# Kernel optimization log

Hardware: AMD Instinct MI355X
Metric: run time of the kernel (lower is better)

Reference implementation:

```python
import jax, jax.numpy as jnp
import numpy as np

D_MODEL = 1024
NUM_HEADS = 16
D_K = D_MODEL // NUM_HEADS
ROPE_THETA = 10000.0
SEQ = 4096


def setup_inputs() -> dict:
    key = jax.random.key(0)
    ks = jax.random.split(key, 5)
    s = 1.0 / np.sqrt(D_MODEL)
    return {
        "x": jax.random.normal(ks[0], (1, SEQ, D_MODEL), jnp.float32),
        "token_positions": jnp.arange(SEQ, dtype=jnp.int32),
        "Wq": jax.random.normal(ks[1], (D_MODEL, D_MODEL), jnp.float32) * s,
        "Wk": jax.random.normal(ks[2], (D_MODEL, D_MODEL), jnp.float32) * s,
        "Wv": jax.random.normal(ks[3], (D_MODEL, D_MODEL), jnp.float32) * s,
        "Wo": jax.random.normal(ks[4], (D_MODEL, D_MODEL), jnp.float32) * s,
    }


def _rope(t, positions):
    # t: [b, h, s, d_k]; interleaved pair rotation
    half = D_K // 2
    inv_freq = ROPE_THETA ** (-jnp.arange(half, dtype=jnp.float32) * 2.0 / D_K)
    ang = positions.astype(jnp.float32)[:, None] * inv_freq[None, :]  # [s, half]
    cos, sin = jnp.cos(ang), jnp.sin(ang)
    x1 = t[..., 0::2]
    x2 = t[..., 1::2]
    r1 = x1 * cos - x2 * sin
    r2 = x1 * sin + x2 * cos
    return jnp.stack([r1, r2], axis=-1).reshape(t.shape)


def reference(x, token_positions, Wq, Wk, Wv, Wo):
    b, s, _ = x.shape
    def split_heads(t):
        return t.reshape(b, s, NUM_HEADS, D_K).transpose(0, 2, 1, 3)  # [b,h,s,dk]
    q = split_heads(x @ Wq.T)
    k = split_heads(x @ Wk.T)
    v = split_heads(x @ Wv.T)
    q = _rope(q, token_positions)
    k = _rope(k, token_positions)
    scores = jnp.einsum('bhqd,bhkd->bhqk', q, k) / np.sqrt(D_K)
    causal = jnp.tril(jnp.ones((s, s), dtype=bool))
    scores = jnp.where(causal, scores, -jnp.inf)
    attn = jax.nn.softmax(scores, axis=-1)
    out = jnp.einsum('bhqk,bhkd->bhqd', attn, v)
    out = out.transpose(0, 2, 1, 3).reshape(b, s, D_MODEL)
    return out @ Wo.T
```

## Files before the change

### kernel.cpp

```cpp
#include <hip/hip_runtime.h>

#define S    4096
#define DM   1024
#define H    16
#define DK   64

typedef __bf16 bf16;
typedef __bf16 bf16x8 __attribute__((ext_vector_type(8)));
typedef __bf16 bf16x4 __attribute__((ext_vector_type(4)));
typedef float  f32x4  __attribute__((ext_vector_type(4)));

__global__ __launch_bounds__(256)
void convert_kernel(const float* __restrict__ x,  const float* __restrict__ wq,
                    const float* __restrict__ wk, const float* __restrict__ wv,
                    const float* __restrict__ wo,
                    bf16* __restrict__ xb,  bf16* __restrict__ wqb,
                    bf16* __restrict__ wkb, bf16* __restrict__ wvb,
                    bf16* __restrict__ wob)
{
    const size_t i = (size_t)blockIdx.x * 256 + threadIdx.x;
    const float* src; bf16* dst; size_t off;
    if (i < 1048576)      { src = x;  dst = xb;  off = i; }
    else if (i < 1310720) { src = wq; dst = wqb; off = i - 1048576; }
    else if (i < 1572864) { src = wk; dst = wkb; off = i - 1310720; }
    else if (i < 1835008) { src = wv; dst = wvb; off = i - 1572864; }
    else                  { src = wo; dst = wob; off = i - 1835008; }
    f32x4 v = ((const f32x4*)src)[off];
    bf16x4 b;
    for (int r = 0; r < 4; r++) b[r] = (bf16)v[r];
    ((bf16x4*)dst)[off] = b;
}

__global__ __launch_bounds__(256)
void gemm_kernel(const bf16* __restrict__ A,
                 const bf16* __restrict__ w0, const bf16* __restrict__ w1,
                 const bf16* __restrict__ w2,
                 const int* __restrict__ pos,
                 bf16* __restrict__ o0, bf16* __restrict__ o1,
                 bf16* __restrict__ o2,
                 float* __restrict__ of,
                 int base_mode)
{
    const int z    = blockIdx.z;
    const int mode = base_mode + z;
    const bf16* W  = (z == 0) ? w0 : (z == 1 ? w1 : w2);
    bf16* Out      = (z == 0) ? o0 : (z == 1 ? o1 : o2);

    __shared__ bf16 As[64 * 72];
    __shared__ bf16 Bs[64 * 72];

    const int tid  = threadIdx.x;
    const int lane = tid & 63;
    const int wv   = tid >> 6;
    const int quad = lane >> 4;
    const int col  = lane & 15;
    const int wm   = wv >> 1, wn = wv & 1;

    const int tileM = blockIdx.x * 64;
    const int tileN = blockIdx.y * 64;

    const int ldRow = tid >> 2;
    const int ldK   = (tid & 3) * 16;

    f32x4 acc[2][2] = {};

    for (int kc = 0; kc < DM; kc += 64) {
        bf16x8 a0 = *(const bf16x8*)&A[(size_t)(tileM + ldRow) * DM + kc + ldK];
        bf16x8 a1 = *(const bf16x8*)&A[(size_t)(tileM + ldRow) * DM + kc + ldK + 8];
        bf16x8 b0 = *(const bf16x8*)&W[(size_t)(tileN + ldRow) * DM + kc + ldK];
        bf16x8 b1 = *(const bf16x8*)&W[(size_t)(tileN + ldRow) * DM + kc + ldK + 8];
        __syncthreads();
        *(bf16x8*)&As[ldRow * 72 + ldK]     = a0;
        *(bf16x8*)&As[ldRow * 72 + ldK + 8] = a1;
        *(bf16x8*)&Bs[ldRow * 72 + ldK]     = b0;
        *(bf16x8*)&Bs[ldRow * 72 + ldK + 8] = b1;
        __syncthreads();

        for (int kk = 0; kk < 2; kk++) {
            bf16x8 af0 = *(const bf16x8*)&As[(wm * 32 + 0 * 16 + col) * 72 + kk * 32 + quad * 8];
            bf16x8 af1 = *(const bf16x8*)&As[(wm * 32 + 1 * 16 + col) * 72 + kk * 32 + quad * 8];
            bf16x8 bf0 = *(const bf16x8*)&Bs[(wn * 32 + 0 * 16 + col) * 72 + kk * 32 + quad * 8];
            bf16x8 bf1 = *(const bf16x8*)&Bs[(wn * 32 + 1 * 16 + col) * 72 + kk * 32 + quad * 8];

            acc[0][0] = __builtin_amdgcn_mfma_f32_16x16x32_bf16(af0, bf0, acc[0][0], 0, 0, 0);
            acc[0][1] = __builtin_amdgcn_mfma_f32_16x16x32_bf16(af0, bf1, acc[0][1], 0, 0, 0);
            acc[1][0] = __builtin_amdgcn_mfma_f32_16x16x32_bf16(af1, bf0, acc[1][0], 0, 0, 0);
            acc[1][1] = __builtin_amdgcn_mfma_f32_16x16x32_bf16(af1, bf1, acc[1][1], 0, 0, 0);
        }
    }

    for (int fm = 0; fm < 2; fm++)
    for (int fn = 0; fn < 2; fn++) {
        f32x4 v = acc[fm][fn];
        const int n = tileN + wn * 32 + fn * 16 + col;
        for (int r = 0; r < 4; r++) {
            const int m = tileM + wm * 32 + fm * 16 + quad * 4 + r;
            float val = v[r];
            if (mode <= 1) {
                float part = __shfl_xor(val, 1);
                const int d = n & 63;
                const int i = d >> 1;
                float inv = exp2f(-(float)i * 0.41524101186092034f);
                float ang = (float)pos[m] * inv;
                float c = cosf(ang), sn = sinf(ang);
                float rot = (n & 1) ? (val * c + part * sn)
                                    : (val * c - part * sn);
                if (mode == 0) rot *= 0.18033688011112042f;
                Out[((size_t)(n >> 6) * S + m) * 64 + d] = (bf16)rot;
            } else if (mode == 2) {
                Out[(size_t)n * S + m] = (bf16)val;
            } else {
                of[(size_t)m * DM + n] = val;
            }
        }
    }
}

__global__ __launch_bounds__(256, 5)
void attn_kernel(const bf16* __restrict__ q, const bf16* __restrict__ k,
                 const bf16* __restrict__ vt,
                 bf16* __restrict__ P0g, bf16* __restrict__ P1g,
                 float* __restrict__ l0g, float* __restrict__ l1g)
{
    const int bx   = blockIdx.x;
    const int qb_  = (bx & 1) ? (63 - (bx >> 1)) : (bx >> 1);
    const int h    = blockIdx.y;
    const int z    = blockIdx.z;
    const int tid  = threadIdx.x;
    const int lane = tid & 63;
    const int wv   = tid >> 6;
    const int quad = lane >> 4;
    const int col  = lane & 15;

    const int nt   = qb_ + 1;
    const int half = (nt + 1) >> 1;
    const int kt0  = z ? half : 0;
    const int kt1  = z ? nt   : half;

    __shared__ bf16 Ks[64 * 72];
    __shared__ bf16 Vs[64 * 72];
    __shared__ bf16 plds[4][16 * 72];

    const int qbase = qb_ * 64 + wv * 16;

    bf16x8 qf0 = *(const bf16x8*)&q[((size_t)(h * S + qbase + col)) * 64 + quad * 8];
    bf16x8 qf1 = *(const bf16x8*)&q[((size_t)(h * S + qbase + col)) * 64 + 32 + quad * 8];

    float li = 0.f;
    f32x4 o[4] = {};
    const int gq = qbase + col;

    const int srow = tid >> 2;
    const int sseg = (tid & 3) * 16;
    const bf16* kg_ = k  + ((size_t)h * S) * 64;
    const bf16* vg_ = vt + ((size_t)h * 64) * S;

    bf16x8 kr0 = *(const bf16x8*)(kg_ + (size_t)(kt0 * 64 + srow) * 64 + sseg);
    bf16x8 kr1 = *(const bf16x8*)(kg_ + (size_t)(kt0 * 64 + srow) * 64 + sseg + 8);
    bf16x8 vr0 = *(const bf16x8*)(vg_ + (size_t)srow * S + kt0 * 64 + sseg);
    bf16x8 vr1 = *(const bf16x8*)(vg_ + (size_t)srow * S + kt0 * 64 + sseg + 8);

    for (int kt = kt0; kt < kt1; kt++) {
        const int kbase = kt * 64;

        __syncthreads();
        *(bf16x8*)&Ks[srow * 72 + sseg]     = kr0;
        *(bf16x8*)&Ks[srow * 72 + sseg + 8] = kr1;
        *(bf16x8*)&Vs[srow * 72 + sseg]     = vr0;
        *(bf16x8*)&Vs[srow * 72 + sseg + 8] = vr1;
        __syncthreads();

        if (kt + 1 < kt1) {
            const int nb = kbase + 64;
            kr0 = *(const bf16x8*)(kg_ + (size_t)(nb + srow) * 64 + sseg);
            kr1 = *(const bf16x8*)(kg_ + (size_t)(nb + srow) * 64 + sseg + 8);
            vr0 = *(const bf16x8*)(vg_ + (size_t)srow * S + nb + sseg);
            vr1 = *(const bf16x8*)(vg_ + (size_t)srow * S + nb + sseg + 8);
        }

        f32x4 st[4];
        __builtin_amdgcn_s_setprio(1);
        for (int kg = 0; kg < 4; kg++) {
            bf16x8 kf0 = *(const bf16x8*)&Ks[(kg * 16 + col) * 72 + quad * 8];
            bf16x8 kf1 = *(const bf16x8*)&Ks[(kg * 16 + col) * 72 + 32 + quad * 8];
            f32x4 zz = {};
            zz = __builtin_amdgcn_mfma_f32_16x16x32_bf16(kf0, qf0, zz, 0, 0, 0);
            zz = __builtin_amdgcn_mfma_f32_16x16x32_bf16(kf1, qf1, zz, 0, 0, 0);
            st[kg] = zz;
        }
        __builtin_amdgcn_s_setprio(0);

        if (kt == qb_) {
            for (int kg = 0; kg < 4; kg++)
                for (int r = 0; r < 4; r++) {
                    const int gk = kbase + kg * 16 + quad * 4 + r;
                    st[kg][r] = (gk > gq) ? -1e30f : st[kg][r];
                }
        }

        float ps = 0.f;
        for (int kg = 0; kg < 4; kg++) {
            bf16x4 pk;
            for (int r = 0; r < 4; r++) {
                float p = exp2f(st[kg][r]);
                ps += p;
                pk[r] = (bf16)p;
            }
            *(bf16x4*)&plds[wv][col * 72 + kg * 16 + quad * 4] = pk;
        }
        ps += __shfl_xor(ps, 16);
        ps += __shfl_xor(ps, 32);
        li += ps;

        __builtin_amdgcn_wave_barrier();

        bf16x8 pb0 = *(const bf16x8*)&plds[wv][col * 72 + quad * 8];
        bf16x8 pb1 = *(const bf16x8*)&plds[wv][col * 72 + 32 + quad * 8];

        __builtin_amdgcn_s_setprio(1);
        for (int dg = 0; dg < 4; dg++) {
            bf16x8 va0 = *(const bf16x8*)&Vs[(dg * 16 + col) * 72 + quad * 8];
            bf16x8 va1 = *(const bf16x8*)&Vs[(dg * 16 + col) * 72 + 32 + quad * 8];
            o[dg] = __builtin_amdgcn_mfma_f32_16x16x32_bf16(va0, pb0, o[dg], 0, 0, 0);
            o[dg] = __builtin_amdgcn_mfma_f32_16x16x32_bf16(va1, pb1, o[dg], 0, 0, 0);
        }
        __builtin_amdgcn_s_setprio(0);
    }

    bf16*  Pz = z ? P1g : P0g;
    float* lz = z ? l1g : l0g;
    for (int dg = 0; dg < 4; dg++) {
        bf16x4 ov;
        for (int r = 0; r < 4; r++) ov[r] = (bf16)o[dg][r];
        *(bf16x4*)&Pz[(size_t)gq * DM + h * 64 + dg * 16 + quad * 4] = ov;
    }
    if (quad == 0) lz[(size_t)h * S + gq] = li;
}

__global__ __launch_bounds__(256)
void combine_kernel(const bf16* __restrict__ P0, const bf16* __restrict__ P1,
                    const float* __restrict__ l0, const float* __restrict__ l1,
                    bf16* __restrict__ ao)
{
    const size_t i    = (size_t)blockIdx.x * 256 + threadIdx.x;
    const size_t base = i * 8;
    const int s  = (int)(base >> 10);
    const int dm = (int)(base & 1023);
    const int h  = dm >> 6;
    const float rli = 1.f / (l0[(size_t)h * S + s] + l1[(size_t)h * S + s]);
    bf16x8 a = *(const bf16x8*)&P0[base];
    bf16x8 b = *(const bf16x8*)&P1[base];
    bf16x8 ov;
    for (int r = 0; r < 8; r++)
        ov[r] = (bf16)(((float)a[r] + (float)b[r]) * rli);
    *(bf16x8*)&ao[base] = ov;
}

extern "C" void kernel_launch(void* const* d_in, const int* in_sizes, int n_in,
                              void* d_out, int out_size, void* d_ws, size_t ws_size,
                              hipStream_t stream)
{
    const float* x   = (const float*)d_in[0];
    const int*   pos = (const int*)d_in[1];
    const float* Wq  = (const float*)d_in[2];
    const float* Wk  = (const float*)d_in[3];
    const float* Wv  = (const float*)d_in[4];
    const float* Wo  = (const float*)d_in[5];
    float* out = (float*)d_out;

    char* w = (char*)d_ws;
    bf16*  xb  = (bf16*)(w);
    bf16*  wqb = (bf16*)(w + (size_t) 8 * 1024 * 1024);
    bf16*  wkb = (bf16*)(w + (size_t)10 * 1024 * 1024);
    bf16*  wvb = (bf16*)(w + (size_t)12 * 1024 * 1024);
    bf16*  P0  = (bf16*)(w);
    bf16*  P1  = (bf16*)(w + (size_t) 8 * 1024 * 1024);
    bf16*  qb  = (bf16*)(w + (size_t)16 * 1024 * 1024);
    bf16*  kb  = (bf16*)(w + (size_t)24 * 1024 * 1024);
    bf16*  vt  = (bf16*)(w + (size_t)32 * 1024 * 1024);
    float* l0  = (float*)(w + (size_t)40 * 1024 * 1024);
    float* l1  = (float*)(w + (size_t)40 * 1024 * 1024 + 256 * 1024);
    bf16*  ao  = (bf16*)(w + (size_t)16 * 1024 * 1024);
    bf16*  wob = (bf16*)(w + (size_t)46 * 1024 * 1024);

    dim3 blk(256);
    convert_kernel<<<dim3(8192), blk, 0, stream>>>(x, Wq, Wk, Wv, Wo,
                                                   xb, wqb, wkb, wvb, wob);
    gemm_kernel<<<dim3(64, 16, 3), blk, 0, stream>>>(xb, wqb, wkb, wvb, pos,
                                                     qb, kb, vt, out, 0);
    attn_kernel<<<dim3(64, 16, 2), blk, 0, stream>>>(qb, kb, vt,
                                                     P0, P1, l0, l1);
    combine_kernel<<<dim3(2048), blk, 0, stream>>>(P0, P1, l0, l1, ao);
    gemm_kernel<<<dim3(64, 16, 1), blk, 0, stream>>>(ao, wob, wob, wob, pos,
                                                     P0, P0, P0, out, 3);
}
```

Baseline: 280.2 us.

## Load K/V fragments directly from global memory and remap attention blocks per XCD

The attention kernel no longer stages K and V tiles through shared memory with block-wide barriers. Each wave now loads its MFMA operand fragments straight from global memory, relying on L2/cache reuse across the four waves. The grid is flattened so that heads map to XCDs for L2 locality, with the longest causal query blocks scheduled first, and occupancy is lowered to 4 blocks per SM. The change also swaps exp2f for raw v_exp_f32 and adds explicit unrolling, but each wave now issues redundant global loads of the same K/V data.

New measurement: 411.7 us. 1.47x slower.

```diff
diff --git a/kernel.cpp b/kernel.cpp
--- a/kernel.cpp
+++ b/kernel.cpp
@@ -116,16 +116,20 @@
     }
 }
 
-__global__ __launch_bounds__(256, 5)
+__global__ __launch_bounds__(256, 4)
 void attn_kernel(const bf16* __restrict__ q, const bf16* __restrict__ k,
                  const bf16* __restrict__ vt,
                  bf16* __restrict__ P0g, bf16* __restrict__ P1g,
                  float* __restrict__ l0g, float* __restrict__ l1g)
 {
-    const int bx   = blockIdx.x;
-    const int qb_  = (bx & 1) ? (63 - (bx >> 1)) : (bx >> 1);
-    const int h    = blockIdx.y;
-    const int z    = blockIdx.z;
+    const int bid  = blockIdx.x;
+    const int xcd  = bid & 7;
+    const int seq  = bid >> 3;
+    const int h    = (xcd << 1) | (seq & 1);
+    const int rest = seq >> 1;
+    const int z    = rest & 1;
+    const int qb_  = 63 - (rest >> 1);
+
     const int tid  = threadIdx.x;
     const int lane = tid & 63;
     const int wv   = tid >> 6;
@@ -137,8 +141,6 @@
     const int kt0  = z ? half : 0;
     const int kt1  = z ? nt   : half;
 
-    __shared__ bf16 Ks[64 * 72];
-    __shared__ bf16 Vs[64 * 72];
     __shared__ bf16 plds[4][16 * 72];
 
     const int qbase = qb_ * 64 + wv * 16;
@@ -150,48 +152,42 @@
     f32x4 o[4] = {};
     const int gq = qbase + col;
 
-    const int srow = tid >> 2;
-    const int sseg = (tid & 3) * 16;
-    const bf16* kg_ = k  + ((size_t)h * S) * 64;
-    const bf16* vg_ = vt + ((size_t)h * 64) * S;
-
-    bf16x8 kr0 = *(const bf16x8*)(kg_ + (size_t)(kt0 * 64 + srow) * 64 + sseg);
-    bf16x8 kr1 = *(const bf16x8*)(kg_ + (size_t)(kt0 * 64 + srow) * 64 + sseg + 8);
-    bf16x8 vr0 = *(const bf16x8*)(vg_ + (size_t)srow * S + kt0 * 64 + sseg);
-    bf16x8 vr1 = *(const bf16x8*)(vg_ + (size_t)srow * S + kt0 * 64 + sseg + 8);
+    const bf16* kp = k  + ((size_t)h * S + (size_t)kt0 * 64 + col) * 64 + quad * 8;
+    const bf16* vp = vt + ((size_t)(h * 64 + col)) * S + (size_t)kt0 * 64 + quad * 8;
 
     for (int kt = kt0; kt < kt1; kt++) {
         const int kbase = kt * 64;
 
-        __syncthreads();
-        *(bf16x8*)&Ks[srow * 72 + sseg]     = kr0;
-        *(bf16x8*)&Ks[srow * 72 + sseg + 8] = kr1;
-        *(bf16x8*)&Vs[srow * 72 + sseg]     = vr0;
-        *(bf16x8*)&Vs[srow * 72 + sseg + 8] = vr1;
-        __syncthreads();
-
-        if (kt + 1 < kt1) {
-            const int nb = kbase + 64;
-            kr0 = *(const bf16x8*)(kg_ + (size_t)(nb + srow) * 64 + sseg);
-            kr1 = *(const bf16x8*)(kg_ + (size_t)(nb + srow) * 64 + sseg + 8);
-            vr0 = *(const bf16x8*)(vg_ + (size_t)srow * S + nb + sseg);
-            vr1 = *(const bf16x8*)(vg_ + (size_t)srow * S + nb + sseg + 8);
-        }
-
+        bf16x8 kf[4][2];
+#pragma unroll
+        for (int kg = 0; kg < 4; kg++) {
+            kf[kg][0] = *(const bf16x8*)(kp + kg * 16 * 64);
+            kf[kg][1] = *(const bf16x8*)(kp + kg * 16 * 64 + 32);
+        }
         f32x4 st[4];
         __builtin_amdgcn_s_setprio(1);
+#pragma unroll
         for (int kg = 0; kg < 4; kg++) {
-            bf16x8 kf0 = *(const bf16x8*)&Ks[(kg * 16 + col) * 72 + quad * 8];
-            bf16x8 kf1 = *(const bf16x8*)&Ks[(kg * 16 + col) * 72 + 32 + quad * 8];
             f32x4 zz = {};
-            zz = __builtin_amdgcn_mfma_f32_16x16x32_bf16(kf0, qf0, zz, 0, 0, 0);
-            zz = __builtin_amdgcn_mfma_f32_16x16x32_bf16(kf1, qf1, zz, 0, 0, 0);
+            zz = __builtin_amdgcn_mfma_f32_16x16x32_bf16(kf[kg][0], qf0, zz, 0, 0, 0);
+            zz = __builtin_amdgcn_mfma_f32_16x16x32_bf16(kf[kg][1], qf1, zz, 0, 0, 0);
             st[kg] = zz;
         }
         __builtin_amdgcn_s_setprio(0);
 
+        bf16x8 vf[4][2];
+#pragma unroll
+        for (int dg = 0; dg < 4; dg++) {
+            vf[dg][0] = *(const bf16x8*)(vp + (size_t)dg * 16 * S);
+            vf[dg][1] = *(const bf16x8*)(vp + (size_t)dg * 16 * S + 32);
+        }
+        kp += 64 * 64;
+        vp += 64;
+
         if (kt == qb_) {
+#pragma unroll
             for (int kg = 0; kg < 4; kg++)
+#pragma unroll
                 for (int r = 0; r < 4; r++) {
                     const int gk = kbase + kg * 16 + quad * 4 + r;
                     st[kg][r] = (gk > gq) ? -1e30f : st[kg][r];
@@ -199,10 +195,13 @@
         }
 
         float ps = 0.f;
+#pragma unroll
         for (int kg = 0; kg < 4; kg++) {
             bf16x4 pk;
+#pragma unroll
             for (int r = 0; r < 4; r++) {
-                float p = exp2f(st[kg][r]);
+                float p;
+                asm("v_exp_f32 %0, %1" : "=v"(p) : "v"(st[kg][r]));
                 ps += p;
                 pk[r] = (bf16)p;
             }
@@ -218,19 +217,20 @@
         bf16x8 pb1 = *(const bf16x8*)&plds[wv][col * 72 + 32 + quad * 8];
 
         __builtin_amdgcn_s_setprio(1);
+#pragma unroll
         for (int dg = 0; dg < 4; dg++) {
-            bf16x8 va0 = *(const bf16x8*)&Vs[(dg * 16 + col) * 72 + quad * 8];
-            bf16x8 va1 = *(const bf16x8*)&Vs[(dg * 16 + col) * 72 + 32 + quad * 8];
-            o[dg] = __builtin_amdgcn_mfma_f32_16x16x32_bf16(va0, pb0, o[dg], 0, 0, 0);
-            o[dg] = __builtin_amdgcn_mfma_f32_16x16x32_bf16(va1, pb1, o[dg], 0, 0, 0);
+            o[dg] = __builtin_amdgcn_mfma_f32_16x16x32_bf16(vf[dg][0], pb0, o[dg], 0, 0, 0);
+            o[dg] = __builtin_amdgcn_mfma_f32_16x16x32_bf16(vf[dg][1], pb1, o[dg], 0, 0, 0);
         }
         __builtin_amdgcn_s_setprio(0);
     }
 
     bf16*  Pz = z ? P1g : P0g;
     float* lz = z ? l1g : l0g;
+#pragma unroll
     for (int dg = 0; dg < 4; dg++) {
         bf16x4 ov;
+#pragma unroll
         for (int r = 0; r < 4; r++) ov[r] = (bf16)o[dg][r];
         *(bf16x4*)&Pz[(size_t)gq * DM + h * 64 + dg * 16 + quad * 4] = ov;
     }
@@ -288,8 +288,8 @@
                                                    xb, wqb, wkb, wvb, wob);
     gemm_kernel<<<dim3(64, 16, 3), blk, 0, stream>>>(xb, wqb, wkb, wvb, pos,
                                                      qb, kb, vt, out, 0);
-    attn_kernel<<<dim3(64, 16, 2), blk, 0, stream>>>(qb, kb, vt,
-                                                     P0, P1, l0, l1);
+    attn_kernel<<<dim3(2048), blk, 0, stream>>>(qb, kb, vt,
+                                                P0, P1, l0, l1);
     combine_kernel<<<dim3(2048), blk, 0, stream>>>(P0, P1, l0, l1, ao);
     gemm_kernel<<<dim3(64, 16, 1), blk, 0, stream>>>(ao, wob, wob, wob, pos,
                                                      P0, P0, P0, out, 3);
```

## Enlarge attention query tile to 256 rows with XCD-aware balanced block mapping

Applied to the files above, without the earlier changes.

The attention kernel now gives each workgroup 256 query rows instead of 64, with each wave handling four 16-row query tiles. Every K/V tile loaded into LDS is therefore reused across four times as many queries, which cuts global and LDS traffic per score. A flat 512-block grid is decoded so that heads map to XCDs, and the key range is split into two equal halves that pair short and long causal blocks for load balance. The softmax exponent uses a raw v_exp_f32 instruction, and launch bounds drop to 2 workgroups per SIMD to make room for the larger register tile, which lowers occupancy.

Result: faster. 230.0 us (-17.9%).

```diff
diff --git a/kernel.cpp b/kernel.cpp
--- a/kernel.cpp
+++ b/kernel.cpp
@@ -116,39 +116,47 @@
     }
 }
 
-__global__ __launch_bounds__(256, 5)
+__global__ __launch_bounds__(256, 2)
 void attn_kernel(const bf16* __restrict__ q, const bf16* __restrict__ k,
                  const bf16* __restrict__ vt,
                  bf16* __restrict__ P0g, bf16* __restrict__ P1g,
                  float* __restrict__ l0g, float* __restrict__ l1g)
 {
-    const int bx   = blockIdx.x;
-    const int qb_  = (bx & 1) ? (63 - (bx >> 1)) : (bx >> 1);
-    const int h    = blockIdx.y;
-    const int z    = blockIdx.z;
+    const int bid = blockIdx.x;
+    const int xcd = bid & 7;
+    const int b3  = (bid >> 3) & 1;
+    const int u   = (bid >> 4) & 15;
+    const int b8  = (bid >> 8) & 1;
+    const int h   = (xcd << 1) | b8;
+    const int z   = b3;
+    const int QB  = (b3 == b8) ? (15 - u) : u;
+
     const int tid  = threadIdx.x;
     const int lane = tid & 63;
     const int wv   = tid >> 6;
     const int quad = lane >> 4;
     const int col  = lane & 15;
 
-    const int nt   = qb_ + 1;
-    const int half = (nt + 1) >> 1;
-    const int kt0  = z ? half : 0;
-    const int kt1  = z ? nt   : half;
+    const int T2  = 2 * QB + 2;
+    const int kt0 = z * T2;
+    const int kt1 = kt0 + T2;
 
     __shared__ bf16 Ks[64 * 72];
     __shared__ bf16 Vs[64 * 72];
-    __shared__ bf16 plds[4][16 * 72];
-
-    const int qbase = qb_ * 64 + wv * 16;
-
-    bf16x8 qf0 = *(const bf16x8*)&q[((size_t)(h * S + qbase + col)) * 64 + quad * 8];
-    bf16x8 qf1 = *(const bf16x8*)&q[((size_t)(h * S + qbase + col)) * 64 + 32 + quad * 8];
-
-    float li = 0.f;
-    f32x4 o[4] = {};
-    const int gq = qbase + col;
+    __shared__ bf16 plds[4][64 * 40];
+
+    const int qbase = QB * 256 + wv * 64;
+
+    bf16x8 qf[4][2];
+#pragma unroll
+    for (int qt = 0; qt < 4; qt++) {
+        const bf16* qr = &q[((size_t)(h * S + qbase + qt * 16 + col)) * 64];
+        qf[qt][0] = *(const bf16x8*)(qr + quad * 8);
+        qf[qt][1] = *(const bf16x8*)(qr + 32 + quad * 8);
+    }
+
+    float li[4] = {};
+    f32x4 o[4][4] = {};
 
     const int srow = tid >> 2;
     const int sseg = (tid & 3) * 16;
@@ -178,63 +186,96 @@
             vr1 = *(const bf16x8*)(vg_ + (size_t)srow * S + nb + sseg + 8);
         }
 
-        f32x4 st[4];
-        __builtin_amdgcn_s_setprio(1);
-        for (int kg = 0; kg < 4; kg++) {
-            bf16x8 kf0 = *(const bf16x8*)&Ks[(kg * 16 + col) * 72 + quad * 8];
-            bf16x8 kf1 = *(const bf16x8*)&Ks[(kg * 16 + col) * 72 + 32 + quad * 8];
-            f32x4 zz = {};
-            zz = __builtin_amdgcn_mfma_f32_16x16x32_bf16(kf0, qf0, zz, 0, 0, 0);
-            zz = __builtin_amdgcn_mfma_f32_16x16x32_bf16(kf1, qf1, zz, 0, 0, 0);
-            st[kg] = zz;
+        const bool diag = (kt >= (QB << 2));
+
+#pragma unroll
+        for (int half = 0; half < 2; half++) {
+            __builtin_amdgcn_wave_barrier();
+#pragma unroll
+            for (int kg2 = 0; kg2 < 2; kg2++) {
+                const int kg = half * 2 + kg2;
+                bf16x8 kf0 = *(const bf16x8*)&Ks[(kg * 16 + col) * 72 + quad * 8];
+                bf16x8 kf1 = *(const bf16x8*)&Ks[(kg * 16 + col) * 72 + 32 + quad * 8];
+
+                f32x4 st[4];
+                __builtin_amdgcn_s_setprio(1);
+#pragma unroll
+                for (int qt = 0; qt < 4; qt++) {
+                    f32x4 zz = {};
+                    zz = __builtin_amdgcn_mfma_f32_16x16x32_bf16(kf0, qf[qt][0], zz, 0, 0, 0);
+                    zz = __builtin_amdgcn_mfma_f32_16x16x32_bf16(kf1, qf[qt][1], zz, 0, 0, 0);
+                    st[qt] = zz;
+                }
+                __builtin_amdgcn_s_setprio(0);
+
+                if (diag) {
+#pragma unroll
+                    for (int qt = 0; qt < 4; qt++) {
+                        const int gq = qbase + qt * 16 + col;
+#pragma unroll
+                        for (int r = 0; r < 4; r++) {
+                            const int gk = kbase + kg * 16 + quad * 4 + r;
+                            st[qt][r] = (gk > gq) ? -1e30f : st[qt][r];
+                        }
+                    }
+                }
+
+#pragma unroll
+                for (int qt = 0; qt < 4; qt++) {
+                    bf16x4 pk;
+#pragma unroll
+                    for (int r = 0; r < 4; r++) {
+                        float p;
+                        asm("v_exp_f32 %0, %1" : "=v"(p) : "v"(st[qt][r]));
+                        li[qt] += p;
+                        pk[r] = (bf16)p;
+                    }
+                    *(bf16x4*)&plds[wv][(qt * 16 + col) * 40 + kg2 * 16 + quad * 4] = pk;
+                }
+            }
+
+            __builtin_amdgcn_wave_barrier();
+
+            bf16x8 pb[4];
+#pragma unroll
+            for (int qt = 0; qt < 4; qt++)
+                pb[qt] = *(const bf16x8*)&plds[wv][(qt * 16 + col) * 40 + quad * 8];
+
+            __builtin_amdgcn_s_setprio(1);
+#pragma unroll
+            for (int dg = 0; dg < 4; dg++) {
+                bf16x8 va = *(const bf16x8*)&Vs[(dg * 16 + col) * 72 + half * 32 + quad * 8];
+#pragma unroll
+                for (int qt = 0; qt < 4; qt++)
+                    o[dg][qt] = __builtin_amdgcn_mfma_f32_16x16x32_bf16(va, pb[qt], o[dg][qt], 0, 0, 0);
+            }
+            __builtin_amdgcn_s_setprio(0);
         }
-        __builtin_amdgcn_s_setprio(0);
-
-        if (kt == qb_) {
-            for (int kg = 0; kg < 4; kg++)
-                for (int r = 0; r < 4; r++) {
-                    const int gk = kbase + kg * 16 + quad * 4 + r;
-                    st[kg][r] = (gk > gq) ? -1e30f : st[kg][r];
-                }
-        }
-
-        float ps = 0.f;
-        for (int kg = 0; kg < 4; kg++) {
-            bf16x4 pk;
-            for (int r = 0; r < 4; r++) {
-                float p = exp2f(st[kg][r]);
-                ps += p;
-                pk[r] = (bf16)p;
-            }
-            *(bf16x4*)&plds[wv][col * 72 + kg * 16 + quad * 4] = pk;
-        }
-        ps += __shfl_xor(ps, 16);
-        ps += __shfl_xor(ps, 32);
-        li += ps;
-
-        __builtin_amdgcn_wave_barrier();
-
-        bf16x8 pb0 = *(const bf16x8*)&plds[wv][col * 72 + quad * 8];
-        bf16x8 pb1 = *(const bf16x8*)&plds[wv][col * 72 + 32 + quad * 8];
-
-        __builtin_amdgcn_s_setprio(1);
-        for (int dg = 0; dg < 4; dg++) {
-            bf16x8 va0 = *(const bf16x8*)&Vs[(dg * 16 + col) * 72 + quad * 8];
-            bf16x8 va1 = *(const bf16x8*)&Vs[(dg * 16 + col) * 72 + 32 + quad * 8];
-            o[dg] = __builtin_amdgcn_mfma_f32_16x16x32_bf16(va0, pb0, o[dg], 0, 0, 0);
-            o[dg] = __builtin_amdgcn_mfma_f32_16x16x32_bf16(va1, pb1, o[dg], 0, 0, 0);
-        }
-        __builtin_amdgcn_s_setprio(0);
+    }
+
+#pragma unroll
+    for (int qt = 0; qt < 4; qt++) {
+        li[qt] += __shfl_xor(li[qt], 16);
+        li[qt] += __shfl_xor(li[qt], 32);
     }
 
     bf16*  Pz = z ? P1g : P0g;
     float* lz = z ? l1g : l0g;
-    for (int dg = 0; dg < 4; dg++) {
+#pragma unroll
+    for (int dg = 0; dg < 4; dg++)
+#pragma unroll
+    for (int qt = 0; qt < 4; qt++) {
+        const int gq = qbase + qt * 16 + col;
         bf16x4 ov;
-        for (int r = 0; r < 4; r++) ov[r] = (bf16)o[dg][r];
+#pragma unroll
+        for (int r = 0; r < 4; r++) ov[r] = (bf16)o[dg][qt][r];
         *(bf16x4*)&Pz[(size_t)gq * DM + h * 64 + dg * 16 + quad * 4] = ov;
     }
-    if (quad == 0) lz[(size_t)h * S + gq] = li;
+    if (quad == 0) {
+#pragma unroll
+        for (int qt = 0; qt < 4; qt++)
+            lz[(size_t)h * S + qbase + qt * 16 + col] = li[qt];
+    }
 }
 
 __global__ __launch_bounds__(256)
@@ -288,8 +329,8 @@
                                                    xb, wqb, wkb, wvb, wob);
     gemm_kernel<<<dim3(64, 16, 3), blk, 0, stream>>>(xb, wqb, wkb, wvb, pos,
                                                      qb, kb, vt, out, 0);
-    attn_kernel<<<dim3(64, 16, 2), blk, 0, stream>>>(qb, kb, vt,
-                                                     P0, P1, l0, l1);
+    attn_kernel<<<dim3(512), blk, 0, stream>>>(qb, kb, vt,
+                                               P0, P1, l0, l1);
     combine_kernel<<<dim3(2048), blk, 0, stream>>>(P0, P1, l0, l1, ao);
     gemm_kernel<<<dim3(64, 16, 1), blk, 0, stream>>>(ao, wob, wob, wob, pos,
                                                      P0, P0, P0, out, 3);
```
